# Kernel optimization log

Hardware: AMD Instinct MI355X
Metric: run time of the kernel (lower is better)

Reference implementation:

```python
import jax, jax.numpy as jnp
import numpy as np

B, H, W, C = 32, 56, 56, 128
WS, NH, DEPTH = 7, 4, 2
SHIFT = WS // 2
N = WS * WS
HID = 4 * C
CPB = 512


def _layernorm(x, g, b, eps=1e-5):
    m = x.mean(-1, keepdims=True)
    v = ((x - m) ** 2).mean(-1, keepdims=True)
    return (x - m) * jax.lax.rsqrt(v + eps) * g + b


def _window_partition(x):
    b, h, w, c = x.shape
    x = x.reshape(b, h // WS, WS, w // WS, WS, c)
    return x.transpose(0, 1, 3, 2, 4, 5).reshape(-1, N, c)


def _window_reverse(xw, h, w):
    c = xw.shape[-1]
    b = xw.shape[0] // ((h // WS) * (w // WS))
    x = xw.reshape(b, h // WS, w // WS, WS, WS, c)
    return x.transpose(0, 1, 3, 2, 4, 5).reshape(b, h, w, c)


def _rel_index():
    coords = np.stack(np.meshgrid(np.arange(WS), np.arange(WS), indexing='ij'))
    flat = coords.reshape(2, -1)
    rel = (flat[:, :, None] - flat[:, None, :]).transpose(1, 2, 0).astype(np.int64)
    rel[..., 0] += WS - 1
    rel[..., 1] += WS - 1
    rel[..., 0] *= 2 * WS - 1
    return jnp.asarray(rel.sum(-1))  # [N, N]


def _coords_table():
    # SwinV2 log-spaced continuous relative coords table (pretrained_window_size=0 path)
    r = np.arange(-(WS - 1), WS, dtype=np.float32)
    t = np.stack(np.meshgrid(r, r, indexing='ij'), axis=-1)  # [2W-1, 2W-1, 2]
    t = t / (WS - 1) * 8.0
    t = np.sign(t) * np.log2(np.abs(t) + 1.0) / np.log2(8.0)
    return jnp.asarray(t.reshape(-1, 2))  # [(2W-1)^2, 2]


def _shift_mask():
    img = np.zeros((H, W), np.float32)
    cnt = 0
    for hs in (slice(0, -WS), slice(-WS, -SHIFT), slice(-SHIFT, None)):
        for ws_ in (slice(0, -WS), slice(-WS, -SHIFT), slice(-SHIFT, None)):
            img[hs, ws_] = cnt
            cnt += 1
    mw = np.asarray(_window_partition(jnp.asarray(img)[None, :, :, None])).reshape(-1, N)
    diff = mw[:, None, :] - mw[:, :, None]
    return jnp.asarray(np.where(diff != 0, -100.0, 0.0).astype(np.float32))  # [nW, N, N]


def _forward(x, qkv_w, q_bias, v_bias, logit_scale, cpb_w1, cpb_b1, cpb_w2,
             proj_w, proj_b, norm1_g, norm1_b, mlp_w1, mlp_b1, mlp_w2, mlp_b2,
             norm2_g, norm2_b, pm_g, pm_b, pm_w):
    rel_idx = _rel_index()
    table = _coords_table()
    smask = _shift_mask()
    for i in range(DEPTH):
        shift = 0 if i % 2 == 0 else SHIFT
        xs = jnp.roll(x, (-shift, -shift), axis=(1, 2)) if shift else x
        xw = _window_partition(xs)  # [B*nW, N, C]
        bias = jnp.concatenate([q_bias[i], jnp.zeros_like(q_bias[i]), v_bias[i]])
        qkv = (xw @ qkv_w[i] + bias).reshape(-1, N, 3, NH, C // NH).transpose(2, 0, 3, 1, 4)
        q, k, v = qkv[0], qkv[1], qkv[2]  # [B*nW, NH, N, hd]
        qn = q / jnp.maximum(jnp.linalg.norm(q, axis=-1, keepdims=True), 1e-12)
        kn = k / jnp.maximum(jnp.linalg.norm(k, axis=-1, keepdims=True), 1e-12)
        scale = jnp.exp(jnp.minimum(logit_scale[i], jnp.log(100.0)))  # [NH,1,1]
        attn = jnp.einsum('bhnd,bhmd->bhnm', qn, kn) * scale
        rpb = 16.0 * jax.nn.sigmoid(
            (jax.nn.relu(table @ cpb_w1[i] + cpb_b1[i]) @ cpb_w2[i])[rel_idx])  # [N,N,NH]
        attn = attn + rpb.transpose(2, 0, 1)[None]
        if shift:
            nW = smask.shape[0]
            attn = (attn.reshape(-1, nW, NH, N, N) + smask[None, :, None]).reshape(-1, NH, N, N)
        attn = jax.nn.softmax(attn, axis=-1)
        out = jnp.einsum('bhnm,bhmd->bnhd', attn, v).reshape(-1, N, C)
        out = out @ proj_w[i] + proj_b[i]
        xs = _window_reverse(out, H, W)
        if shift:
            xs = jnp.roll(xs, (shift, shift), axis=(1, 2))
        # SwinV2 post-norm residuals
        x = x + _layernorm(xs, norm1_g[i], norm1_b[i])
        y = jax.nn.gelu(x @ mlp_w1[i] + mlp_b1[i], approximate=False) @ mlp_w2[i] + mlp_b2[i]
        x = x + _layernorm(y, norm2_g[i], norm2_b[i])
    # PatchMerging: [B,H,W,C] -> [B,H/2,W/2,4C] -> norm -> Linear(4C,2C)
    xm = x.reshape(B, H // 2, 2, W // 2, 2, C).transpose(0, 1, 3, 2, 4, 5)
    xm = xm.reshape(B, H // 2, W // 2, 4 * C)
    return _layernorm(xm, pm_g, pm_b) @ pm_w


def setup_inputs() -> dict:
    key = jax.random.key(0)
    ks = jax.random.split(key, 8)
    s = 0.02
    rn = lambda k, shp: jax.random.normal(k, shp, jnp.float32) * s
    return dict(
        x=jax.random.normal(ks[0], (B, H, W, C), jnp.float32),
        qkv_w=rn(ks[1], (DEPTH, C, 3 * C)),
        q_bias=jnp.zeros((DEPTH, C), jnp.float32),
        v_bias=jnp.zeros((DEPTH, C), jnp.float32),
        logit_scale=jnp.full((DEPTH, NH, 1, 1), np.log(10.0), jnp.float32),
        cpb_w1=rn(ks[2], (DEPTH, 2, CPB)),
        cpb_b1=jnp.zeros((DEPTH, CPB), jnp.float32),
        cpb_w2=rn(ks[3], (DEPTH, CPB, NH)),
        proj_w=rn(ks[4], (DEPTH, C, C)),
        proj_b=jnp.zeros((DEPTH, C), jnp.float32),
        norm1_g=jnp.ones((DEPTH, C), jnp.float32),
        norm1_b=jnp.zeros((DEPTH, C), jnp.float32),
        mlp_w1=rn(ks[5], (DEPTH, C, HID)),
        mlp_b1=jnp.zeros((DEPTH, HID), jnp.float32),
        mlp_w2=rn(ks[6], (DEPTH, HID, C)),
        mlp_b2=jnp.zeros((DEPTH, C), jnp.float32),
        norm2_g=jnp.ones((DEPTH, C), jnp.float32),
        norm2_b=jnp.zeros((DEPTH, C), jnp.float32),
        pm_g=jnp.ones((4 * C,), jnp.float32),
        pm_b=jnp.zeros((4 * C,), jnp.float32),
        pm_w=rn(ks[7], (4 * C, 2 * C)),
    )


def reference(x, qkv_w, q_bias, v_bias, logit_scale, cpb_w1, cpb_b1, cpb_w2,
              proj_w, proj_b, norm1_g, norm1_b, mlp_w1, mlp_b1, mlp_w2, mlp_b2,
              norm2_g, norm2_b, pm_g, pm_b, pm_w):
    return _forward(x, qkv_w, q_bias, v_bias, logit_scale, cpb_w1, cpb_b1, cpb_w2,
                    proj_w, proj_b, norm1_g, norm1_b, mlp_w1, mlp_b1, mlp_w2, mlp_b2,
                    norm2_g, norm2_b, pm_g, pm_b, pm_w)
```

## Files before the change

kernel.cpp:

```cpp
#include <hip/hip_runtime.h>
#include <math.h>


namespace {
constexpr int kTok = 32 * 56 * 56;
}

typedef __attribute__((ext_vector_type(8))) short bf16x8;
typedef __attribute__((ext_vector_type(4))) float f32x4;

union FragU {
    int4 i4;
    bf16x8 b8;
    unsigned short u[8];
};

__device__ __forceinline__ short f2bf(float f) {
    unsigned u = __float_as_uint(f);
    return (short)((u + 0x7FFFu + ((u >> 16) & 1u)) >> 16);
}
__device__ __forceinline__ float bf2f(unsigned short u) {
    return __uint_as_float(((unsigned)u) << 16);
}
__device__ __forceinline__ unsigned cvt_pk_bf16(float a, float b) {
    unsigned r;
    asm("v_cvt_pk_bf16_f32 %0, %1, %2" : "=v"(r) : "v"(a), "v"(b));
    return r;
}
__device__ __forceinline__ float gelu_t(float x) {
    float x2 = x * x;
    float t0 = fmaf(0.044715f * x2, x, x);
    float e = exp2f(2.3022227f * t0);
    float r = __builtin_amdgcn_rcpf(e + 1.0f);
    return fmaf(-x, r, x);
}

__global__ __launch_bounds__(256) void k_cpb(
    const float* __restrict__ w1, const float* __restrict__ b1,
    const float* __restrict__ w2, float* __restrict__ out169) {
    int L = blockIdx.x / 169;
    int t = blockIdx.x % 169;
    const float* w1L = w1 + L * 1024;
    const float* b1L = b1 + L * 512;
    const float* w2L = w2 + L * 2048;
    float* outL = out169 + L * 704;
    int ia = t / 13, ib = t % 13;
    float r0 = (float)(ia - 6) * (8.0f / 6.0f);
    float s0 = (r0 > 0.f) ? 1.f : (r0 < 0.f ? -1.f : 0.f);
    float t0 = s0 * log2f(fabsf(r0) + 1.0f) * (1.0f / 3.0f);
    float r1 = (float)(ib - 6) * (8.0f / 6.0f);
    float s1 = (r1 > 0.f) ? 1.f : (r1 < 0.f ? -1.f : 0.f);
    float t1 = s1 * log2f(fabsf(r1) + 1.0f) * (1.0f / 3.0f);

    int tid = threadIdx.x;
    float p0 = 0, p1 = 0, p2 = 0, p3 = 0;
    for (int c = tid; c < 512; c += 256) {
        float hv = fmaxf(t0 * w1L[c] + t1 * w1L[512 + c] + b1L[c], 0.0f);
        p0 += hv * w2L[c * 4 + 0];
        p1 += hv * w2L[c * 4 + 1];
        p2 += hv * w2L[c * 4 + 2];
        p3 += hv * w2L[c * 4 + 3];
    }
    __shared__ float red[256][4];
    red[tid][0] = p0; red[tid][1] = p1; red[tid][2] = p2; red[tid][3] = p3;
    __syncthreads();
    for (int s = 128; s > 0; s >>= 1) {
        if (tid < s) {
            red[tid][0] += red[tid + s][0];
            red[tid][1] += red[tid + s][1];
            red[tid][2] += red[tid + s][2];
            red[tid][3] += red[tid + s][3];
        }
        __syncthreads();
    }
    if (tid < 4) outL[t * 4 + tid] = red[0][tid];
}

__global__ void k_rpb(const float* __restrict__ out169, float* __restrict__ rpb64) {
    int e2 = blockIdx.x * 256 + threadIdx.x;
    int L = e2 >> 14, e = e2 & 16383;
    int h = e >> 12, r = e & 4095;
    int i = r >> 6, j = r & 63;
    float val;
    if (j >= 49) {
        val = -30000.0f;
    } else if (i >= 49) {
        val = 0.0f;
    } else {
        int dp = i / 7 - j / 7 + 6;
        int dq = i % 7 - j % 7 + 6;
        float v = out169[L * 704 + (dp * 13 + dq) * 4 + h];
        val = 16.0f / (1.0f + expf(-v));
    }
    rpb64[e2] = val;
}

__device__ __forceinline__ void cvt_slot(
    const float* __restrict__ W, short* __restrict__ Wb, int slt, int Kb, int N) {
    int nn = slt & 63;
    int tmp = slt >> 6;
    int kb = tmp % Kb;
    int nt = tmp / Kb;
    int n = nt * 64 + nn;
    int k0 = kb * 8;
    union { int4 i4; short s8[8]; } u;
#pragma unroll
    for (int e = 0; e < 8; ++e) u.s8[e] = f2bf(W[(size_t)(k0 + e) * N + n]);
    int nns = (nn & ~3) | ((nn ^ kb) & 3);
    *(int4*)(Wb + (((size_t)tmp) * 64 + nns) * 8) = u.i4;
}

__global__ __launch_bounds__(256) void k_cvtall(
    const float* __restrict__ qkv_w, const float* __restrict__ proj_w,
    const float* __restrict__ mw1, const float* __restrict__ mw2,
    const float* __restrict__ pmw, const float* __restrict__ qb,
    const float* __restrict__ vb, short* __restrict__ wall,
    float* __restrict__ bias384) {
    int s = blockIdx.x * 256 + threadIdx.x;
    short* wqkvb  = wall;
    short* wprojb = wall + 98304;
    short* wm1b   = wall + 131072;
    short* wm2b   = wall + 262144;
    short* wpmb   = wall + 393216;
    if (s < 12288) {
        int L = s / 6144, r = s % 6144;
        cvt_slot(qkv_w + L * 49152, wqkvb + L * 49152, r, 16, 384);
    } else if (s < 16384) {
        int s2 = s - 12288;
        int L = s2 / 2048, r = s2 % 2048;
        cvt_slot(proj_w + L * 16384, wprojb + L * 16384, r, 16, 128);
    } else if (s < 32768) {
        int s2 = s - 16384;
        int L = s2 / 8192, r = s2 % 8192;
        cvt_slot(mw1 + L * 65536, wm1b + L * 65536, r, 16, 512);
    } else if (s < 49152) {
        int s2 = s - 32768;
        int L = s2 / 8192, r = s2 % 8192;
        cvt_slot(mw2 + L * 65536, wm2b + L * 65536, r, 64, 128);
    } else if (s < 65536) {
        cvt_slot(pmw, wpmb, s - 49152, 64, 256);
    } else if (s < 66304) {
        int t = s - 65536;
        int L = t / 384, f = t % 384;
        float v = (f < 128) ? qb[L * 128 + f]
                            : ((f < 256) ? 0.0f : vb[L * 128 + f - 256]);
        bias384[t] = v;
    }
}

__global__ __launch_bounds__(256) void k_cvtx(
    const float* __restrict__ x, short* __restrict__ xb) {
    size_t e = ((size_t)blockIdx.x * 256 + threadIdx.x) * 8;
    const float* src = x + e;
    float4 f0 = *(const float4*)src;
    float4 f1 = *(const float4*)(src + 4);
    union { int4 i4; short s8[8]; } u;
    u.s8[0] = f2bf(f0.x); u.s8[1] = f2bf(f0.y);
    u.s8[2] = f2bf(f0.z); u.s8[3] = f2bf(f0.w);
    u.s8[4] = f2bf(f1.x); u.s8[5] = f2bf(f1.y);
    u.s8[6] = f2bf(f1.z); u.s8[7] = f2bf(f1.w);
    *(int4*)(xb + e) = u.i4;
}

template <int K, int NT>
__global__ __launch_bounds__(256) void k_gemm(
    const short* __restrict__ Ain, const short* __restrict__ Wb,
    float* __restrict__ Out, int ostride) {
    constexpr int Kb = K / 8;
    constexpr int NC = K / 128;
    __shared__ int4 As4[2048];
    __shared__ int4 Ws4[1024];
    int tid = threadIdx.x;
    int nwg = gridDim.x;
    int chunk = nwg >> 3;
    int lid = (blockIdx.x & 7) * chunk + (blockIdx.x >> 3);
    int mt = lid / NT, nt = lid - mt * NT;
    int mb = mt * 128;
    int w = tid >> 6, l = tid & 63, lr = l & 15, lg = l >> 4;
    const f32x4 fz = {0.f, 0.f, 0.f, 0.f};
    f32x4 acc[2][4];
#pragma unroll
    for (int mi = 0; mi < 2; ++mi)
#pragma unroll
        for (int ni = 0; ni < 4; ++ni) acc[mi][ni] = fz;

    for (int c = 0; c < NC; ++c) {
        if (c) __syncthreads();
#pragma unroll
        for (int it = 0; it < 8; ++it) {
            int s = it * 256 + tid;
            int m = s >> 4, kb = s & 15;
            int slot = kb * 128 + ((m & ~7) | ((m ^ kb) & 7));
            As4[slot] = *(const int4*)(Ain + (size_t)(mb + m) * K + c * 128 + kb * 8);
        }
        {
            const int4* wsrc = (const int4*)(Wb + ((size_t)nt * Kb + c * 16) * 64 * 8);
#pragma unroll
            for (int it = 0; it < 4; ++it) Ws4[it * 256 + tid] = wsrc[it * 256 + tid];
        }
        __syncthreads();
#pragma unroll
        for (int kk = 0; kk < 4; ++kk) {
            int kbl = kk * 4 + lg;
            int m0 = w * 32 + lr;
            bf16x8 a0 = *(const bf16x8*)&As4[kbl * 128 + ((m0 & ~7) | ((m0 ^ kbl) & 7))];
            int m1 = m0 + 16;
            bf16x8 a1 = *(const bf16x8*)&As4[kbl * 128 + ((m1 & ~7) | ((m1 ^ kbl) & 7))];
#pragma unroll
            for (int ni = 0; ni < 4; ++ni) {
                int nn = lr + 16 * ni;
                bf16x8 bfr = *(const bf16x8*)&Ws4[kbl * 64 + ((nn & ~3) | ((nn ^ kbl) & 3))];
                acc[0][ni] = __builtin_amdgcn_mfma_f32_16x16x32_bf16(a0, bfr, acc[0][ni], 0, 0, 0);
                acc[1][ni] = __builtin_amdgcn_mfma_f32_16x16x32_bf16(a1, bfr, acc[1][ni], 0, 0, 0);
            }
        }
    }
#pragma unroll
    for (int ni = 0; ni < 4; ++ni) {
        int col = nt * 64 + ni * 16 + lr;
#pragma unroll
        for (int mi = 0; mi < 2; ++mi) {
#pragma unroll
            for (int r = 0; r < 4; ++r) {
                int row = mb + w * 32 + mi * 16 + lg * 4 + r;
                Out[(size_t)row * ostride + col] = acc[mi][ni][r];
            }
        }
    }
}

template <int K, bool RF32>
__global__ __launch_bounds__(256) void k_gemm_ln(
    const short* __restrict__ Ain, const short* __restrict__ Wb,
    const float* __restrict__ bias, const float* __restrict__ g,
    const float* __restrict__ bt, const void* __restrict__ resid,
    short* __restrict__ xoutb, int shift) {
    constexpr int Kb = K / 8;
    constexpr int NC = K / 128;
    __shared__ int4 As4[1024];
    __shared__ int4 Ws4[2048];
    int tid = threadIdx.x;
    int mb = blockIdx.x * 64;
    int w = tid >> 6, l = tid & 63, lr = l & 15, lg = l >> 4;
    const f32x4 fz = {0.f, 0.f, 0.f, 0.f};
    f32x4 acc[8];
#pragma unroll
    for (int ni = 0; ni < 8; ++ni) acc[ni] = fz;

    for (int c = 0; c < NC; ++c) {
        if (c) __syncthreads();
#pragma unroll
        for (int it = 0; it < 4; ++it) {
            int s = it * 256 + tid;
            int m = s >> 4, kb = s & 15;
            int slot = kb * 64 + ((m & ~7) | ((m ^ kb) & 7));
            As4[slot] = *(const int4*)(Ain + (size_t)(mb + m) * K + c * 128 + kb * 8);
        }
        {
            const int4* w0 = (const int4*)(Wb + ((size_t)(c * 16)) * 64 * 8);
            const int4* w1 = (const int4*)(Wb + ((size_t)(Kb + c * 16)) * 64 * 8);
#pragma unroll
            for (int it = 0; it < 4; ++it) {
                Ws4[it * 256 + tid] = w0[it * 256 + tid];
                Ws4[1024 + it * 256 + tid] = w1[it * 256 + tid];
            }
        }
        __syncthreads();
#pragma unroll
        for (int kk = 0; kk < 4; ++kk) {
            int kbl = kk * 4 + lg;
            int m0 = w * 16 + lr;
            bf16x8 a0 = *(const bf16x8*)&As4[kbl * 64 + ((m0 & ~7) | ((m0 ^ kbl) & 7))];
#pragma unroll
            for (int ni = 0; ni < 8; ++ni) {
                int nn = lr + 16 * (ni & 3);
                bf16x8 bfr = *(const bf16x8*)&Ws4[(ni >> 2) * 1024 + kbl * 64 +
                                                  ((nn & ~3) | ((nn ^ kbl) & 3))];
                acc[ni] = __builtin_amdgcn_mfma_f32_16x16x32_bf16(a0, bfr, acc[ni], 0, 0, 0);
            }
        }
    }
    float bv[8], gv[8], btv[8];
#pragma unroll
    for (int ni = 0; ni < 8; ++ni) {
        int col = ni * 16 + lr;
        bv[ni] = bias[col]; gv[ni] = g[col]; btv[ni] = bt[col];
    }
#pragma unroll
    for (int r = 0; r < 4; ++r) {
        int row = mb + w * 16 + lg * 4 + r;
        float v[8];
        float s1 = 0.f, s2 = 0.f;
#pragma unroll
        for (int ni = 0; ni < 8; ++ni) {
            v[ni] = acc[ni][r] + bv[ni];
            s1 += v[ni];
            s2 = fmaf(v[ni], v[ni], s2);
        }
#pragma unroll
        for (int off = 8; off >= 1; off >>= 1) {
            s1 += __shfl_xor(s1, off);
            s2 += __shfl_xor(s2, off);
        }
        float mean = s1 * (1.0f / 128.0f);
        float var = s2 * (1.0f / 128.0f) - mean * mean;
        float rstd = rsqrtf(var + 1e-5f);
        int mo = row;
        if (shift) {
            int b = row / 3136, rr = row % 3136;
            int hh = rr / 56 + shift; if (hh >= 56) hh -= 56;
            int ww = rr % 56 + shift; if (ww >= 56) ww -= 56;
            mo = b * 3136 + hh * 56 + ww;
        }
        size_t base = (size_t)mo * 128;
#pragma unroll
        for (int ni = 0; ni < 8; ++ni) {
            int col = ni * 16 + lr;
            float rv = RF32 ? ((const float*)resid)[base + col]
                            : bf2f(((const unsigned short*)resid)[base + col]);
            float o = rv + (v[ni] - mean) * rstd * gv[ni] + btv[ni];
            xoutb[base + col] = f2bf(o);
        }
    }
}

__global__ __launch_bounds__(512) void k_mlp(
    short* __restrict__ xb, const short* __restrict__ W1b,
    const short* __restrict__ W2b, const float* __restrict__ b1,
    const float* __restrict__ b2, const float* __restrict__ g,
    const float* __restrict__ bt) {
    __shared__ int4 W1s[1024];
    __shared__ int4 W2s[1024];
    __shared__ short Hs[8 * 1152];
    int tid = threadIdx.x;
    int mb = blockIdx.x * 128;
    int w = tid >> 6, l = tid & 63, lr = l & 15, lg = l >> 4;
    const f32x4 fz = {0.f, 0.f, 0.f, 0.f};
    short* Hw = Hs + w * 1152;

    int4 xfrag[4];
#pragma unroll
    for (int kk = 0; kk < 4; ++kk)
        xfrag[kk] = *(const int4*)(
            xb + (size_t)(mb + w * 16 + lr) * 128 + kk * 32 + lg * 8);

    f32x4 acc2[8];
#pragma unroll
    for (int ni = 0; ni < 8; ++ni) acc2[ni] = fz;

    for (int c = 0; c < 8; ++c) {
        __syncthreads();
        {
            const int4* w1src = (const int4*)(W1b + (size_t)c * 8192);
#pragma unroll
            for (int it = 0; it < 2; ++it) W1s[it * 512 + tid] = w1src[it * 512 + tid];
            const int4* w2a = (const int4*)(W2b + (size_t)(c * 8) * 512);
            const int4* w2c = (const int4*)(W2b + (size_t)(64 + c * 8) * 512);
            W2s[tid] = w2a[tid];
            W2s[512 + tid] = w2c[tid];
        }
        __syncthreads();
        f32x4 a1[4];
#pragma unroll
        for (int ct = 0; ct < 4; ++ct) a1[ct] = fz;
        __builtin_amdgcn_s_setprio(1);
#pragma unroll
        for (int kk = 0; kk < 4; ++kk) {
            int kbl = kk * 4 + lg;
            FragU xa; xa.i4 = xfrag[kk];
#pragma unroll
            for (int ct = 0; ct < 4; ++ct) {
                int nn = lr + 16 * ct;
                bf16x8 w1f = *(const bf16x8*)&W1s[kbl * 64 + ((nn & ~3) | ((nn ^ kbl) & 3))];
                a1[ct] = __builtin_amdgcn_mfma_f32_16x16x32_bf16(w1f, xa.b8, a1[ct], 0, 0, 0);
            }
        }
        __builtin_amdgcn_s_setprio(0);
#pragma unroll
        for (int ct = 0; ct < 4; ++ct) {
            float4 bb = *(const float4*)(b1 + c * 64 + ct * 16 + lg * 4);
            float h0 = gelu_t(a1[ct][0] + bb.x);
            float h1 = gelu_t(a1[ct][1] + bb.y);
            float h2 = gelu_t(a1[ct][2] + bb.z);
            float h3 = gelu_t(a1[ct][3] + bb.w);
            unsigned p0 = cvt_pk_bf16(h0, h1);
            unsigned p1 = cvt_pk_bf16(h2, h3);
            *(int2*)&Hw[lr * 72 + ct * 16 + lg * 4] = make_int2((int)p0, (int)p1);
        }
        __builtin_amdgcn_s_setprio(1);
#pragma unroll
        for (int kc = 0; kc < 2; ++kc) {
            int kbl = kc * 4 + lg;
            FragU ha; ha.i4 = *(const int4*)&Hw[lr * 72 + kc * 32 + lg * 8];
#pragma unroll
            for (int ni = 0; ni < 8; ++ni) {
                int nn = lr + 16 * (ni & 3);
                bf16x8 w2f = *(const bf16x8*)&W2s[(ni >> 2) * 512 + kbl * 64 +
                                                  ((nn & ~3) | ((nn ^ kbl) & 3))];
                acc2[ni] = __builtin_amdgcn_mfma_f32_16x16x32_bf16(ha.b8, w2f, acc2[ni], 0, 0, 0);
            }
        }
        __builtin_amdgcn_s_setprio(0);
    }

    float bv[8], gv[8], btv[8];
#pragma unroll
    for (int ni = 0; ni < 8; ++ni) {
        int col = ni * 16 + lr;
        bv[ni] = b2[col]; gv[ni] = g[col]; btv[ni] = bt[col];
    }
#pragma unroll
    for (int r = 0; r < 4; ++r) {
        int row = mb + w * 16 + lg * 4 + r;
        float v[8];
        float s1 = 0.f, s2 = 0.f;
#pragma unroll
        for (int ni = 0; ni < 8; ++ni) {
            v[ni] = acc2[ni][r] + bv[ni];
            s1 += v[ni];
            s2 = fmaf(v[ni], v[ni], s2);
        }
#pragma unroll
        for (int off = 8; off >= 1; off >>= 1) {
            s1 += __shfl_xor(s1, off);
            s2 += __shfl_xor(s2, off);
        }
        float mean = s1 * (1.0f / 128.0f);
        float var = s2 * (1.0f / 128.0f) - mean * mean;
        float rstd = rsqrtf(var + 1e-5f);
        size_t base = (size_t)row * 128;
#pragma unroll
        for (int ni = 0; ni < 8; ++ni) {
            int col = ni * 16 + lr;
            float rv = bf2f(((const unsigned short*)xb)[base + col]);
            float o = rv + (v[ni] - mean) * rstd * gv[ni] + btv[ni];
            xb[base + col] = f2bf(o);
        }
    }
}

__global__ __launch_bounds__(256) void k_attn(
    const short* __restrict__ xb, const short* __restrict__ Wq,
    const float* __restrict__ bias384, const float* __restrict__ rpb64,
    const float* __restrict__ ls, short* __restrict__ aout, int shift) {
    __shared__ short qkvs[64 * 264];
    __shared__ short Vth[4 * 2304];
    int wid = blockIdx.x;
    int b = wid >> 6, wrem = wid & 63;
    int wh = wrem >> 3, ww_ = wrem & 7;
    int tid = threadIdx.x;
    int w = tid >> 6;
    int l = tid & 63, lr = l & 15, lg = l >> 4;
    int tokbase = b * 3136 + wh * 7 * 56 + ww_ * 7;
    const f32x4 fz = {0.f, 0.f, 0.f, 0.f};

    {
        int ti = w * 16 + lr;
        bool valid = (ti < 49);
        int4 xfrag[4];
        const int4 zero4 = make_int4(0, 0, 0, 0);
        if (valid) {
            int m = tokbase + (ti / 7) * 56 + (ti % 7);
            if (shift) {
                int bb2 = m / 3136, rr = m % 3136;
                int hh = rr / 56 + shift; if (hh >= 56) hh -= 56;
                int ww2 = rr % 56 + shift; if (ww2 >= 56) ww2 -= 56;
                m = bb2 * 3136 + hh * 56 + ww2;
            }
#pragma unroll
            for (int kk = 0; kk < 4; ++kk)
                xfrag[kk] = *(const int4*)(xb + (size_t)m * 128 + kk * 32 + lg * 8);
        } else {
#pragma unroll
            for (int kk = 0; kk < 4; ++kk) xfrag[kk] = zero4;
        }
        short* orow = qkvs + (w * 16 + lr) * 264;
#pragma unroll
        for (int ft = 0; ft < 24; ++ft) {
            f32x4 a = fz;
            int n = ft * 16 + lr;
            int nt = n >> 6, nn = n & 63;
#pragma unroll
            for (int kk = 0; kk < 4; ++kk) {
                int kbl = kk * 4 + lg;
                int nns = (nn & ~3) | ((nn ^ kbl) & 3);
                bf16x8 wf = *(const bf16x8*)(Wq + (((size_t)nt * 16 + kbl) * 64 + nns) * 8);
                FragU xa; xa.i4 = xfrag[kk];
                a = __builtin_amdgcn_mfma_f32_16x16x32_bf16(wf, xa.b8, a, 0, 0, 0);
            }
            float4 bb = *(const float4*)(bias384 + ft * 16 + lg * 4);
            if (ft < 16) {
                unsigned p0 = cvt_pk_bf16(a[0] + bb.x, a[1] + bb.y);
                unsigned p1 = cvt_pk_bf16(a[2] + bb.z, a[3] + bb.w);
                *(int2*)&orow[ft * 16 + lg * 4] = make_int2((int)p0, (int)p1);
            } else {
                int f = ft - 16;
                int h2 = f >> 1;
                int dbase = (f & 1) * 16 + lg * 4;
                int tok = w * 16 + lr;
                short* vdst = Vth + h2 * 2304 + dbase * 72 + tok;
                float av[4] = {a[0] + bb.x, a[1] + bb.y, a[2] + bb.z, a[3] + bb.w};
#pragma unroll
                for (int r = 0; r < 4; ++r) vdst[r * 72] = f2bf(av[r]);
            }
        }
    }
    __syncthreads();

    int h = w;
    short* Vt = Vth + h * 2304;

    float scale = __expf(fminf(ls[h], 4.6051702f));
    int4 qf[4], kf[4];
#pragma unroll
    for (int t = 0; t < 4; ++t) {
        const short* base = qkvs + (t * 16 + lr) * 264 + h * 32 + lg * 8;
        qf[t] = *(const int4*)base;
        kf[t] = *(const int4*)(base + 128);
    }
    __syncthreads();
    short* Pt = qkvs + h * 1152;

    float invq[4], ikreg[4];
#pragma unroll
    for (int t = 0; t < 4; ++t) {
        {
            FragU u; u.i4 = qf[t];
            float ss = 0.f;
#pragma unroll
            for (int e = 0; e < 8; ++e) { float x = bf2f(u.u[e]); ss = fmaf(x, x, ss); }
            ss += __shfl_xor(ss, 16);
            ss += __shfl_xor(ss, 32);
            invq[t] = scale / fmaxf(sqrtf(ss), 1e-12f);
        }
        {
            FragU u; u.i4 = kf[t];
            float ss = 0.f;
#pragma unroll
            for (int e = 0; e < 8; ++e) { float x = bf2f(u.u[e]); ss = fmaf(x, x, ss); }
            ss += __shfl_xor(ss, 16);
            ss += __shfl_xor(ss, 32);
            ikreg[t] = 1.0f / fmaxf(sqrtf(ss), 1e-12f);
        }
    }
    float ika[4][4];
#pragma unroll
    for (int jt = 0; jt < 4; ++jt)
#pragma unroll
        for (int r = 0; r < 4; ++r)
            ika[jt][r] = __shfl(ikreg[jt], lg * 4 + r);

    bool edge = (shift != 0) && ((wh == 7) || (ww_ == 7));
    const float* rbase = rpb64 + h * 4096;
    f32x4 oacc[2][4];
#pragma unroll
    for (int mi = 0; mi < 2; ++mi)
#pragma unroll
        for (int ni = 0; ni < 4; ++ni) oacc[mi][ni] = fz;

#pragma unroll
    for (int qt = 0; qt < 4; ++qt) {
        f32x4 at[4];
        __builtin_amdgcn_s_setprio(1);
#pragma unroll
        for (int jt = 0; jt < 4; ++jt) {
            FragU a; a.i4 = kf[jt];
            FragU bq; bq.i4 = qf[qt];
            at[jt] = __builtin_amdgcn_mfma_f32_16x16x32_bf16(a.b8, bq.b8, fz, 0, 0, 0);
        }
        __builtin_amdgcn_s_setprio(0);

        float iq = invq[qt];
        int qi = qt * 16 + lr;
        int qc = (qi < 49) ? qi : 48;
        int rlq = 0, clq = 0;
        if (edge) {
            rlq = (wh == 7) ? ((qc / 7) < 4 ? 1 : 2) : 0;
            clq = (ww_ == 7) ? ((qc % 7) < 4 ? 1 : 2) : 0;
        }
#pragma unroll
        for (int jt = 0; jt < 4; ++jt) {
            float4 rv = *(const float4*)(rbase + qc * 64 + jt * 16 + lg * 4);
            float rr[4] = {rv.x, rv.y, rv.z, rv.w};
#pragma unroll
            for (int r = 0; r < 4; ++r) {
                float v = fmaf(at[jt][r] * ika[jt][r], iq, rr[r]);
                if (edge) {
                    int j = jt * 16 + lg * 4 + r;
                    int jc = (j < 49) ? j : 48;
                    int rlk = (wh == 7) ? ((jc / 7) < 4 ? 1 : 2) : 0;
                    int clk = (ww_ == 7) ? ((jc % 7) < 4 ? 1 : 2) : 0;
                    if (rlk != rlq || clk != clq) v -= 100.0f;
                }
                at[jt][r] = v;
            }
        }
        float m = -1e30f;
#pragma unroll
        for (int jt = 0; jt < 4; ++jt)
#pragma unroll
            for (int r = 0; r < 4; ++r) m = fmaxf(m, at[jt][r]);
        m = fmaxf(m, __shfl_xor(m, 16));
        m = fmaxf(m, __shfl_xor(m, 32));
        float s = 0.f;
#pragma unroll
        for (int jt = 0; jt < 4; ++jt)
#pragma unroll
            for (int r = 0; r < 4; ++r) {
                float p = __expf(at[jt][r] - m);
                at[jt][r] = p;
                s += p;
            }
        s += __shfl_xor(s, 16);
        s += __shfl_xor(s, 32);
        float inv = 1.0f / s;
#pragma unroll
        for (int jt = 0; jt < 4; ++jt) {
            unsigned lo = cvt_pk_bf16(at[jt][0] * inv, at[jt][1] * inv);
            unsigned hi = cvt_pk_bf16(at[jt][2] * inv, at[jt][3] * inv);
            *(int2*)&Pt[lr * 72 + jt * 16 + lg * 4] = make_int2((int)lo, (int)hi);
        }
        __builtin_amdgcn_s_setprio(1);
#pragma unroll
        for (int kc = 0; kc < 2; ++kc) {
            FragU pb;
            pb.i4 = *(const int4*)&Pt[lr * 72 + kc * 32 + lg * 8];
#pragma unroll
            for (int mi = 0; mi < 2; ++mi) {
                FragU va;
                va.i4 = *(const int4*)&Vt[(mi * 16 + lr) * 72 + kc * 32 + lg * 8];
                oacc[mi][qt] = __builtin_amdgcn_mfma_f32_16x16x32_bf16(
                    va.b8, pb.b8, oacc[mi][qt], 0, 0, 0);
            }
        }
        __builtin_amdgcn_s_setprio(0);
    }

#pragma unroll
    for (int ni = 0; ni < 4; ++ni) {
        int qrow = ni * 16 + lr;
        if (qrow < 49) {
            int tok = tokbase + (qrow / 7) * 56 + (qrow % 7);
#pragma unroll
            for (int mi = 0; mi < 2; ++mi) {
                unsigned lo = cvt_pk_bf16(oacc[mi][ni][0], oacc[mi][ni][1]);
                unsigned hi = cvt_pk_bf16(oacc[mi][ni][2], oacc[mi][ni][3]);
                *(int2*)&aout[(size_t)tok * 128 + h * 32 + mi * 16 + lg * 4] =
                    make_int2((int)lo, (int)hi);
            }
        }
    }
}

__global__ __launch_bounds__(256) void k_pmln(
    const short* __restrict__ x, const float* __restrict__ g,
    const float* __restrict__ bt, short* __restrict__ outb) {
    int m2 = blockIdx.x * 4 + (threadIdx.x >> 6);
    int l = threadIdx.x & 63;
    int b = m2 / 784, r = m2 % 784;
    int h2 = r / 28, w2 = r % 28;
    int q0 = l * 8;
    int i2 = q0 >> 8, j2 = (q0 >> 7) & 1, c = q0 & 127;
    const short* src = x + (size_t)((b * 56 + 2 * h2 + i2) * 56 + 2 * w2 + j2) * 128 + c;
    FragU u; u.i4 = *(const int4*)src;
    float v[8];
#pragma unroll
    for (int e = 0; e < 8; ++e) v[e] = bf2f(u.u[e]);
    float s1 = 0.f, s2 = 0.f;
#pragma unroll
    for (int e = 0; e < 8; ++e) { s1 += v[e]; s2 = fmaf(v[e], v[e], s2); }
#pragma unroll
    for (int off = 32; off >= 1; off >>= 1) {
        s1 += __shfl_xor(s1, off);
        s2 += __shfl_xor(s2, off);
    }
    float mean = s1 * (1.0f / 512.0f);
    float var = s2 * (1.0f / 512.0f) - mean * mean;
    float rstd = rsqrtf(var + 1e-5f);
    union { int4 i4; short s8[8]; } o;
#pragma unroll
    for (int e = 0; e < 8; ++e)
        o.s8[e] = f2bf((v[e] - mean) * rstd * g[q0 + e] + bt[q0 + e]);
    *(int4*)(outb + (size_t)m2 * 512 + q0) = o.i4;
}

extern "C" void kernel_launch(void* const* d_in, const int* in_sizes, int n_in,
                              void* d_out, int out_size, void* d_ws, size_t ws_size,
                              hipStream_t stream) {
    const float* x_in   = (const float*)d_in[0];
    const float* qkv_w  = (const float*)d_in[1];
    const float* q_bias = (const float*)d_in[2];
    const float* v_bias = (const float*)d_in[3];
    const float* lscale = (const float*)d_in[4];
    const float* cpb_w1 = (const float*)d_in[5];
    const float* cpb_b1 = (const float*)d_in[6];
    const float* cpb_w2 = (const float*)d_in[7];
    const float* proj_w = (const float*)d_in[8];
    const float* proj_b = (const float*)d_in[9];
    const float* n1g    = (const float*)d_in[10];
    const float* n1b    = (const float*)d_in[11];
    const float* mw1    = (const float*)d_in[12];
    const float* mb1    = (const float*)d_in[13];
    const float* mw2    = (const float*)d_in[14];
    const float* mb2    = (const float*)d_in[15];
    const float* n2g    = (const float*)d_in[16];
    const float* n2b    = (const float*)d_in[17];
    const float* pmg    = (const float*)d_in[18];
    const float* pmb    = (const float*)d_in[19];
    const float* pmw    = (const float*)d_in[20];
    float* out = (float*)d_out;

    float* wsf    = (float*)d_ws;
    short* wall   = (short*)wsf;
    short* wqkvb  = wall;
    short* wprojb = wall + 98304;
    short* wm1b   = wall + 131072;
    short* wm2b   = wall + 262144;
    short* wpmb   = wall + 393216;
    float* out169 = wsf + 262144;
    float* rpb64  = out169 + 1408;
    float* bias384 = rpb64 + 32768;

    float* R1      = wsf + (size_t)12845056;
    short* attnout = (short*)(R1 + (size_t)19267584);
    short* pmin    = (short*)R1;
    short* xb      = (short*)(R1 + (size_t)25690112);

    k_cvtall<<<260, 256, 0, stream>>>(qkv_w, proj_w, mw1, mw2, pmw,
                                      q_bias, v_bias, wall, bias384);
    k_cpb<<<338, 256, 0, stream>>>(cpb_w1, cpb_b1, cpb_w2, out169);
    k_rpb<<<128, 256, 0, stream>>>(out169, rpb64);
    k_cvtx<<<6272, 256, 0, stream>>>(x_in, xb);

    for (int i = 0; i < 2; ++i) {
        int shift = i ? 3 : 0;
        k_attn<<<2048, 256, 0, stream>>>(
            xb, wqkvb + i * 49152, bias384 + i * 384, rpb64 + i * 16384,
            lscale + i * 4, attnout, shift);
        if (i == 0) {
            k_gemm_ln<128, true><<<1568, 256, 0, stream>>>(
                attnout, wprojb, proj_b, n1g, n1b, x_in, xb, shift);
        } else {
            k_gemm_ln<128, false><<<1568, 256, 0, stream>>>(
                attnout, wprojb + 16384, proj_b + 128, n1g + 128, n1b + 128,
                xb, xb, shift);
        }
        k_mlp<<<784, 512, 0, stream>>>(
            xb, wm1b + i * 65536, wm2b + i * 65536, mb1 + i * 512,
            mb2 + i * 128, n2g + i * 128, n2b + i * 128);
    }
    k_pmln<<<6272, 256, 0, stream>>>(xb, pmg, pmb, pmin);
    k_gemm<512, 4><<<784, 256, 0, stream>>>(pmin, wpmb, out, 256);
}
```

Before: 323.5 us.

## Split attention work across eight waves per window block

The attention kernel now launches 512 threads per window instead of 256. The two halves of the block each compute half of the QKV projection tiles, and then each handle half of the query tiles for their head. This shortens each wave's serial chain and raises the number of resident waves per CU under the same shared-memory footprint. In exchange, K fragments and K norms are loaded and computed redundantly by both halves, and register limits tighten under the larger launch bound.

After: 335.4 us. +3.7%, slower.

```diff
diff --git a/kernel.cpp b/kernel.cpp
--- a/kernel.cpp
+++ b/kernel.cpp
@@ -439,7 +439,7 @@
     }
 }
 
-__global__ __launch_bounds__(256) void k_attn(
+__global__ __launch_bounds__(512) void k_attn(
     const short* __restrict__ xb, const short* __restrict__ Wq,
     const float* __restrict__ bias384, const float* __restrict__ rpb64,
     const float* __restrict__ ls, short* __restrict__ aout, int shift) {
@@ -453,9 +453,10 @@
     int l = tid & 63, lr = l & 15, lg = l >> 4;
     int tokbase = b * 3136 + wh * 7 * 56 + ww_ * 7;
     const f32x4 fz = {0.f, 0.f, 0.f, 0.f};
+    int wg4 = w & 3, whalf = w >> 2;
 
     {
-        int ti = w * 16 + lr;
+        int ti = wg4 * 16 + lr;
         bool valid = (ti < 49);
         int4 xfrag[4];
         const int4 zero4 = make_int4(0, 0, 0, 0);
@@ -474,9 +475,10 @@
 #pragma unroll
             for (int kk = 0; kk < 4; ++kk) xfrag[kk] = zero4;
         }
-        short* orow = qkvs + (w * 16 + lr) * 264;
-#pragma unroll
-        for (int ft = 0; ft < 24; ++ft) {
+        short* orow = qkvs + (wg4 * 16 + lr) * 264;
+#pragma unroll
+        for (int ft2 = 0; ft2 < 12; ++ft2) {
+            int ft = whalf * 12 + ft2;
             f32x4 a = fz;
             int n = ft * 16 + lr;
             int nt = n >> 6, nn = n & 63;
@@ -497,7 +499,7 @@
                 int f = ft - 16;
                 int h2 = f >> 1;
                 int dbase = (f & 1) * 16 + lg * 4;
-                int tok = w * 16 + lr;
+                int tok = wg4 * 16 + lr;
                 short* vdst = Vth + h2 * 2304 + dbase * 72 + tok;
                 float av[4] = {a[0] + bb.x, a[1] + bb.y, a[2] + bb.z, a[3] + bb.w};
 #pragma unroll
@@ -507,41 +509,44 @@
     }
     __syncthreads();
 
-    int h = w;
+    int h = wg4, qh = whalf;
     short* Vt = Vth + h * 2304;
 
     float scale = __expf(fminf(ls[h], 4.6051702f));
-    int4 qf[4], kf[4];
+    int4 qf[2], kf[4];
+#pragma unroll
+    for (int t = 0; t < 2; ++t) {
+        const short* base = qkvs + ((qh * 2 + t) * 16 + lr) * 264 + h * 32 + lg * 8;
+        qf[t] = *(const int4*)base;
+    }
 #pragma unroll
     for (int t = 0; t < 4; ++t) {
         const short* base = qkvs + (t * 16 + lr) * 264 + h * 32 + lg * 8;
-        qf[t] = *(const int4*)base;
         kf[t] = *(const int4*)(base + 128);
     }
     __syncthreads();
-    short* Pt = qkvs + h * 1152;
-
-    float invq[4], ikreg[4];
+    short* Pt = qkvs + w * 1152;
+
+    float invq[2], ikreg[4];
+#pragma unroll
+    for (int t = 0; t < 2; ++t) {
+        FragU u; u.i4 = qf[t];
+        float ss = 0.f;
+#pragma unroll
+        for (int e = 0; e < 8; ++e) { float x = bf2f(u.u[e]); ss = fmaf(x, x, ss); }
+        ss += __shfl_xor(ss, 16);
+        ss += __shfl_xor(ss, 32);
+        invq[t] = scale / fmaxf(sqrtf(ss), 1e-12f);
+    }
 #pragma unroll
     for (int t = 0; t < 4; ++t) {
-        {
-            FragU u; u.i4 = qf[t];
-            float ss = 0.f;
-#pragma unroll
-            for (int e = 0; e < 8; ++e) { float x = bf2f(u.u[e]); ss = fmaf(x, x, ss); }
-            ss += __shfl_xor(ss, 16);
-            ss += __shfl_xor(ss, 32);
-            invq[t] = scale / fmaxf(sqrtf(ss), 1e-12f);
-        }
-        {
-            FragU u; u.i4 = kf[t];
-            float ss = 0.f;
-#pragma unroll
-            for (int e = 0; e < 8; ++e) { float x = bf2f(u.u[e]); ss = fmaf(x, x, ss); }
-            ss += __shfl_xor(ss, 16);
-            ss += __shfl_xor(ss, 32);
-            ikreg[t] = 1.0f / fmaxf(sqrtf(ss), 1e-12f);
-        }
+        FragU u; u.i4 = kf[t];
+        float ss = 0.f;
+#pragma unroll
+        for (int e = 0; e < 8; ++e) { float x = bf2f(u.u[e]); ss = fmaf(x, x, ss); }
+        ss += __shfl_xor(ss, 16);
+        ss += __shfl_xor(ss, 32);
+        ikreg[t] = 1.0f / fmaxf(sqrtf(ss), 1e-12f);
     }
     float ika[4][4];
 #pragma unroll
@@ -552,25 +557,26 @@
 
     bool edge = (shift != 0) && ((wh == 7) || (ww_ == 7));
     const float* rbase = rpb64 + h * 4096;
-    f32x4 oacc[2][4];
+    f32x4 oacc[2][2];
 #pragma unroll
     for (int mi = 0; mi < 2; ++mi)
 #pragma unroll
-        for (int ni = 0; ni < 4; ++ni) oacc[mi][ni] = fz;
-
-#pragma unroll
-    for (int qt = 0; qt < 4; ++qt) {
+        for (int ni = 0; ni < 2; ++ni) oacc[mi][ni] = fz;
+
+#pragma unroll
+    for (int qt2 = 0; qt2 < 2; ++qt2) {
+        int qt = qh * 2 + qt2;
         f32x4 at[4];
         __builtin_amdgcn_s_setprio(1);
 #pragma unroll
         for (int jt = 0; jt < 4; ++jt) {
             FragU a; a.i4 = kf[jt];
-            FragU bq; bq.i4 = qf[qt];
+            FragU bq; bq.i4 = qf[qt2];
             at[jt] = __builtin_amdgcn_mfma_f32_16x16x32_bf16(a.b8, bq.b8, fz, 0, 0, 0);
         }
         __builtin_amdgcn_s_setprio(0);
 
-        float iq = invq[qt];
+        float iq = invq[qt2];
         int qi = qt * 16 + lr;
         int qc = (qi < 49) ? qi : 48;
         int rlq = 0, clq = 0;
@@ -629,22 +635,22 @@
             for (int mi = 0; mi < 2; ++mi) {
                 FragU va;
                 va.i4 = *(const int4*)&Vt[(mi * 16 + lr) * 72 + kc * 32 + lg * 8];
-                oacc[mi][qt] = __builtin_amdgcn_mfma_f32_16x16x32_bf16(
-                    va.b8, pb.b8, oacc[mi][qt], 0, 0, 0);
+                oacc[mi][qt2] = __builtin_amdgcn_mfma_f32_16x16x32_bf16(
+                    va.b8, pb.b8, oacc[mi][qt2], 0, 0, 0);
             }
         }
         __builtin_amdgcn_s_setprio(0);
     }
 
 #pragma unroll
-    for (int ni = 0; ni < 4; ++ni) {
-        int qrow = ni * 16 + lr;
+    for (int qt2 = 0; qt2 < 2; ++qt2) {
+        int qrow = (qh * 2 + qt2) * 16 + lr;
         if (qrow < 49) {
             int tok = tokbase + (qrow / 7) * 56 + (qrow % 7);
 #pragma unroll
             for (int mi = 0; mi < 2; ++mi) {
-                unsigned lo = cvt_pk_bf16(oacc[mi][ni][0], oacc[mi][ni][1]);
-                unsigned hi = cvt_pk_bf16(oacc[mi][ni][2], oacc[mi][ni][3]);
+                unsigned lo = cvt_pk_bf16(oacc[mi][qt2][0], oacc[mi][qt2][1]);
+                unsigned hi = cvt_pk_bf16(oacc[mi][qt2][2], oacc[mi][qt2][3]);
                 *(int2*)&aout[(size_t)tok * 128 + h * 32 + mi * 16 + lg * 4] =
                     make_int2((int)lo, (int)hi);
             }
@@ -734,7 +740,7 @@
 
     for (int i = 0; i < 2; ++i) {
         int shift = i ? 3 : 0;
-        k_attn<<<2048, 256, 0, stream>>>(
+        k_attn<<<2048, 512, 0, stream>>>(
             xb, wqkvb + i * 49152, bias384 + i * 384, rpb64 + i * 16384,
             lscale + i * 4, attnout, shift);
         if (i == 0) {
```

## Split QKV projection across waves by output column instead of token rows

Applied to the files above, without the earlier changes.

Each wave used to compute all 24 output column tiles for its own 16 tokens, so every wave loaded the full QKV weight matrix. Now each wave loads all 64 token rows of x into registers and computes only 6 column tiles for all four token groups. Each weight fragment is reused across four MFMAs, cutting weight loads per wave by a factor of four. The cost is four times the x-fragment registers and redundant x loads in every wave, which raises register pressure and may lower occupancy.

New measurement: 324.6 us. Within noise of the previous version (+0.3%).

```diff
diff --git a/kernel.cpp b/kernel.cpp
--- a/kernel.cpp
+++ b/kernel.cpp
@@ -455,29 +455,33 @@
     const f32x4 fz = {0.f, 0.f, 0.f, 0.f};
 
     {
-        int ti = w * 16 + lr;
-        bool valid = (ti < 49);
-        int4 xfrag[4];
+        int4 xfrag[4][4];
         const int4 zero4 = make_int4(0, 0, 0, 0);
-        if (valid) {
-            int m = tokbase + (ti / 7) * 56 + (ti % 7);
-            if (shift) {
-                int bb2 = m / 3136, rr = m % 3136;
-                int hh = rr / 56 + shift; if (hh >= 56) hh -= 56;
-                int ww2 = rr % 56 + shift; if (ww2 >= 56) ww2 -= 56;
-                m = bb2 * 3136 + hh * 56 + ww2;
-            }
-#pragma unroll
-            for (int kk = 0; kk < 4; ++kk)
-                xfrag[kk] = *(const int4*)(xb + (size_t)m * 128 + kk * 32 + lg * 8);
-        } else {
-#pragma unroll
-            for (int kk = 0; kk < 4; ++kk) xfrag[kk] = zero4;
-        }
-        short* orow = qkvs + (w * 16 + lr) * 264;
-#pragma unroll
-        for (int ft = 0; ft < 24; ++ft) {
-            f32x4 a = fz;
+#pragma unroll
+        for (int tg = 0; tg < 4; ++tg) {
+            int ti = tg * 16 + lr;
+            if (ti < 49) {
+                int m = tokbase + (ti / 7) * 56 + (ti % 7);
+                if (shift) {
+                    int bb2 = m / 3136, rr = m % 3136;
+                    int hh = rr / 56 + shift; if (hh >= 56) hh -= 56;
+                    int ww2 = rr % 56 + shift; if (ww2 >= 56) ww2 -= 56;
+                    m = bb2 * 3136 + hh * 56 + ww2;
+                }
+#pragma unroll
+                for (int kk = 0; kk < 4; ++kk)
+                    xfrag[tg][kk] = *(const int4*)(xb + (size_t)m * 128 + kk * 32 + lg * 8);
+            } else {
+#pragma unroll
+                for (int kk = 0; kk < 4; ++kk) xfrag[tg][kk] = zero4;
+            }
+        }
+#pragma unroll
+        for (int ft2 = 0; ft2 < 6; ++ft2) {
+            int ft = w * 6 + ft2;
+            f32x4 a[4];
+#pragma unroll
+            for (int tg = 0; tg < 4; ++tg) a[tg] = fz;
             int n = ft * 16 + lr;
             int nt = n >> 6, nn = n & 63;
 #pragma unroll
@@ -485,23 +489,33 @@
                 int kbl = kk * 4 + lg;
                 int nns = (nn & ~3) | ((nn ^ kbl) & 3);
                 bf16x8 wf = *(const bf16x8*)(Wq + (((size_t)nt * 16 + kbl) * 64 + nns) * 8);
-                FragU xa; xa.i4 = xfrag[kk];
-                a = __builtin_amdgcn_mfma_f32_16x16x32_bf16(wf, xa.b8, a, 0, 0, 0);
+#pragma unroll
+                for (int tg = 0; tg < 4; ++tg) {
+                    FragU xa; xa.i4 = xfrag[tg][kk];
+                    a[tg] = __builtin_amdgcn_mfma_f32_16x16x32_bf16(wf, xa.b8, a[tg], 0, 0, 0);
+                }
             }
             float4 bb = *(const float4*)(bias384 + ft * 16 + lg * 4);
             if (ft < 16) {
-                unsigned p0 = cvt_pk_bf16(a[0] + bb.x, a[1] + bb.y);
-                unsigned p1 = cvt_pk_bf16(a[2] + bb.z, a[3] + bb.w);
-                *(int2*)&orow[ft * 16 + lg * 4] = make_int2((int)p0, (int)p1);
+#pragma unroll
+                for (int tg = 0; tg < 4; ++tg) {
+                    unsigned p0 = cvt_pk_bf16(a[tg][0] + bb.x, a[tg][1] + bb.y);
+                    unsigned p1 = cvt_pk_bf16(a[tg][2] + bb.z, a[tg][3] + bb.w);
+                    *(int2*)&qkvs[(tg * 16 + lr) * 264 + ft * 16 + lg * 4] =
+                        make_int2((int)p0, (int)p1);
+                }
             } else {
                 int f = ft - 16;
                 int h2 = f >> 1;
                 int dbase = (f & 1) * 16 + lg * 4;
-                int tok = w * 16 + lr;
-                short* vdst = Vth + h2 * 2304 + dbase * 72 + tok;
-                float av[4] = {a[0] + bb.x, a[1] + bb.y, a[2] + bb.z, a[3] + bb.w};
-#pragma unroll
-                for (int r = 0; r < 4; ++r) vdst[r * 72] = f2bf(av[r]);
+#pragma unroll
+                for (int tg = 0; tg < 4; ++tg) {
+                    short* vdst = Vth + h2 * 2304 + dbase * 72 + tg * 16 + lr;
+                    float av[4] = {a[tg][0] + bb.x, a[tg][1] + bb.y,
+                                   a[tg][2] + bb.z, a[tg][3] + bb.w};
+#pragma unroll
+                    for (int r = 0; r < 4; ++r) vdst[r * 72] = f2bf(av[r]);
+                }
             }
         }
     }
```
